# Kernel optimization log

Measured on AMD Instinct MI355X. Metric: run time of the kernel, lower is better.

Reference implementation:

```python
import jax, jax.numpy as jnp
import numpy as np
from jax import lax

WIN = 9
EPS = 1e-05


def _box_sum(v, win):
    # v: [B, 1, D, H, W]
    pad = win // 2
    dn = lax.conv_dimension_numbers(v.shape, (1, 1, win, win, win), ('NCDHW', 'OIDHW', 'NCDHW'))
    k = jnp.ones((win,), v.dtype)
    # apply 1D sum along D, H, W in turn
    v = lax.conv_general_dilated(v, k.reshape(1, 1, win, 1, 1), (1, 1, 1), [(pad, pad), (0, 0), (0, 0)], dimension_numbers=dn)
    v = lax.conv_general_dilated(v, k.reshape(1, 1, 1, win, 1), (1, 1, 1), [(0, 0), (pad, pad), (0, 0)], dimension_numbers=dn)
    v = lax.conv_general_dilated(v, k.reshape(1, 1, 1, 1, win), (1, 1, 1), [(0, 0), (0, 0), (pad, pad)], dimension_numbers=dn)
    return v


def setup_inputs() -> dict:
    key = jax.random.key(0)
    k1, k2 = jax.random.split(key)
    shape = (2, 1, 160, 192, 160)
    x = jax.random.uniform(k1, shape, dtype=jnp.float32)
    y = jax.random.uniform(k2, shape, dtype=jnp.float32)
    return {"x": x, "y": y}


def reference(x, y):
    win = WIN
    win_size = float(win ** 3)
    x_sum = _box_sum(x, win)
    y_sum = _box_sum(y, win)
    x2_sum = _box_sum(x * x, win)
    y2_sum = _box_sum(y * y, win)
    xy_sum = _box_sum(x * y, win)
    cross = xy_sum - x_sum * y_sum / win_size
    x_var = jnp.maximum(x2_sum - x_sum * x_sum / win_size, EPS)
    y_var = jnp.maximum(y2_sum - y_sum * y_sum / win_size, EPS)
    cc = cross * cross / (x_var * y_var)
    return -jnp.mean(cc)
```

## Files before the change

kernel.cpp:

```cpp
#include <hip/hip_runtime.h>

#define BB 2
#define DD 160
#define HH 192
#define WW 160
#define HW (HH * WW)
#define PAD 4
#define TH 16
#define TW 16
#define EXT 24
#define XSTR 28
#define PLANE 768
#define SLOTS (EXT * XSTR)
#define WCS 456
#define WJS 28
#define HCS 272
#define HHS 17
#define CHUNK 28
#define NCH 6
#define NITER 36
#define WT (WW / TW)
#define HT (HH / TH)
#define NBLK (WT * HT * NCH * BB)
#define EPS 1e-5f
#define INV_WS (1.0f / 729.0f)

__device__ __forceinline__ void bar_lgkm() {
  asm volatile("s_waitcnt lgkmcnt(0)" ::: "memory");
  __builtin_amdgcn_s_barrier();
  asm volatile("" ::: "memory");
}

__global__ void __launch_bounds__(256) k_lncc(
    const float* __restrict__ x, const float* __restrict__ y,
    float* __restrict__ partials)
{
  __shared__ float sbuf[2][2][PLANE];
  __shared__ float wsum[5 * WCS];
  __shared__ float hsum[5 * HCS];
  __shared__ float red[4];

  const int t = threadIdx.x;
  const int w0 = blockIdx.x * TW;
  const int h0 = blockIdx.y * TH;
  const int bz = blockIdx.z;
  const int b = bz / NCH;
  const int chunk = bz - b * NCH;
  const int dc0 = chunk * CHUNK;

  int off[3]; float msk[3];
#pragma unroll
  for (int k = 0; k < 3; ++k) {
    int s = t + 256 * k;
    int r = s / XSTR, cl = s - r * XSTR;
    int gh = h0 - PAD + r, gw = w0 - PAD + cl;
    bool ok = (s < SLOTS) & (cl < EXT) &
              ((unsigned)gh < (unsigned)HH) & ((unsigned)gw < (unsigned)WW);
    off[k] = ok ? (gh * WW + gw) : 0;
    msk[k] = ok ? 1.0f : 0.0f;
  }

  const int c2 = t / 24, r2 = t - c2 * 24;
  const bool aIsY = (c2 == 1) | (c2 == 3);
  const bool bIsX = (c2 == 2);
  const bool useB = (c2 >= 2);
  const int paOff = (aIsY ? PLANE : 0) + r2 * XSTR;
  const int pbOff = (bIsX ? 0 : PLANE) + r2 * XSTR;
  float* const wwr = &wsum[c2 * WCS + r2];

  const int c3 = t / 16, w3 = t - c3 * 16;
  const float* const wrd = &wsum[c3 * WCS + w3 * WJS];
  float* const hwr = &hsum[c3 * HCS + w3];

  const int h4 = t >> 4, w4 = t & 15;
  const float* const hrd = &hsum[h4 * HHS + w4];

  const float* xb = x + (long)b * DD * HW;
  const float* yb = y + (long)b * DD * HW;

  float ring[9][5];
#pragma unroll
  for (int i = 0; i < 9; ++i)
#pragma unroll
    for (int c = 0; c < 5; ++c) ring[i][c] = 0.f;
  float run0 = 0.f, run1 = 0.f, run2 = 0.f, run3 = 0.f, run4 = 0.f, acc = 0.f;

  const int g0 = dc0 - PAD;

  float vx0 = 0.f, vx1 = 0.f, vx2 = 0.f, vy0 = 0.f, vy1 = 0.f, vy2 = 0.f;
  if (g0 >= 0) {
    const float* xsl = xb + (long)g0 * HW;
    const float* ysl = yb + (long)g0 * HW;
    vx0 = xsl[off[0]]; vx1 = xsl[off[1]]; vx2 = xsl[off[2]];
    vy0 = ysl[off[0]]; vy1 = ysl[off[1]]; vy2 = ysl[off[2]];
  }

  for (int ito = 0; ito < NITER; ito += 9) {
#pragma unroll
    for (int jj = 0; jj < 9; ++jj) {
      const int it = ito + jj;
      const int g = g0 + it;
      const int p = it & 1;
      const bool gv = (g >= 0) && (g < DD);
      float hv0 = 0.f, hv1 = 0.f, hv2 = 0.f, hv3 = 0.f, hv4 = 0.f;

      if (gv) {
        float* xd = &sbuf[p][0][0];
        float* yd = &sbuf[p][1][0];
        xd[t]       = vx0 * msk[0];
        yd[t]       = vy0 * msk[0];
        xd[t + 256] = vx1 * msk[1];
        yd[t + 256] = vy1 * msk[1];
        xd[t + 512] = vx2 * msk[2];
        yd[t + 512] = vy2 * msk[2];
      }
      {
        const int gn = g + 1;
        if ((gn >= 0) && (gn < DD) && (it + 1 < NITER)) {
          const float* xsl = xb + (long)gn * HW;
          const float* ysl = yb + (long)gn * HW;
          vx0 = xsl[off[0]]; vx1 = xsl[off[1]]; vx2 = xsl[off[2]];
          vy0 = ysl[off[0]]; vy1 = ysl[off[1]]; vy2 = ysl[off[2]];
        }
      }

      if (gv) {
        bar_lgkm();
        if (t < 120) {
          const int pbase = p * (2 * PLANE);
          const float* pa = &sbuf[0][0][0] + pbase + paOff;
          const float* pb = &sbuf[0][0][0] + pbase + pbOff;
          float q[EXT];
#pragma unroll
          for (int i = 0; i < EXT; ++i) {
            float a = pa[i];
            float bv = pb[i];
            q[i] = useB ? a * bv : a;
          }
          float s = ((q[0] + q[1]) + (q[2] + q[3])) +
                    ((q[4] + q[5]) + (q[6] + q[7])) + q[8];
          wwr[0] = s;
#pragma unroll
          for (int j = 1; j < TW; ++j) {
            s += q[j + 8] - q[j - 1];
            wwr[j * WJS] = s;
          }
        }
        bar_lgkm();
        if (t < 80) {
          float v[EXT];
#pragma unroll
          for (int i = 0; i < EXT; ++i) v[i] = wrd[i];
          float s = ((v[0] + v[1]) + (v[2] + v[3])) +
                    ((v[4] + v[5]) + (v[6] + v[7])) + v[8];
          hwr[0] = s;
#pragma unroll
          for (int h = 1; h < TH; ++h) {
            s += v[h + 8] - v[h - 1];
            hwr[h * HHS] = s;
          }
        }
        bar_lgkm();
        hv0 = hrd[0];
        hv1 = hrd[HCS];
        hv2 = hrd[2 * HCS];
        hv3 = hrd[3 * HCS];
        hv4 = hrd[4 * HCS];
      }

      run0 += hv0 - ring[jj][0]; ring[jj][0] = hv0;
      run1 += hv1 - ring[jj][1]; ring[jj][1] = hv1;
      run2 += hv2 - ring[jj][2]; ring[jj][2] = hv2;
      run3 += hv3 - ring[jj][3]; ring[jj][3] = hv3;
      run4 += hv4 - ring[jj][4]; ring[jj][4] = hv4;

      if (it >= 8) {
        const int d = g - PAD;
        if (d < DD) {
          float cross = fmaf(-run0 * INV_WS, run1, run4);
          float xv = fmaxf(fmaf(-run0 * INV_WS, run0, run2), EPS);
          float yv = fmaxf(fmaf(-run1 * INV_WS, run1, run3), EPS);
          acc += (cross * cross) * __builtin_amdgcn_rcpf(xv * yv);
        }
      }
    }
  }

#pragma unroll
  for (int o = 32; o > 0; o >>= 1) acc += __shfl_down(acc, o);
  if ((t & 63) == 0) red[t >> 6] = acc;
  __syncthreads();
  if (t == 0) {
    int bid = (bz * HT + blockIdx.y) * WT + blockIdx.x;
    partials[bid] = (red[0] + red[1]) + (red[2] + red[3]);
  }
}

__global__ void __launch_bounds__(256) k_finalize(
    const float* __restrict__ partials, float* __restrict__ out)
{
  __shared__ double red[256];
  double s = 0.0;
  for (int i = threadIdx.x; i < NBLK; i += 256) s += (double)partials[i];
  red[threadIdx.x] = s;
  __syncthreads();
  for (int o = 128; o > 0; o >>= 1) {
    if (threadIdx.x < o) red[threadIdx.x] += red[threadIdx.x + o];
    __syncthreads();
  }
  if (threadIdx.x == 0) {
    const double Nvox = (double)BB * DD * HH * WW;
    out[0] = (float)(-red[0] / Nvox);
  }
}

extern "C" void kernel_launch(void* const* d_in, const int* in_sizes, int n_in,
                              void* d_out, int out_size, void* d_ws, size_t ws_size,
                              hipStream_t stream) {
  (void)in_sizes; (void)n_in; (void)out_size; (void)ws_size;
  const float* x = (const float*)d_in[0];
  const float* y = (const float*)d_in[1];
  float* out = (float*)d_out;
  float* partials = (float*)d_ws;

  dim3 grid(WT, HT, BB * NCH);
  k_lncc<<<grid, 256, 0, stream>>>(x, y, partials);
  k_finalize<<<1, 256, 0, stream>>>(partials, out);
}
```

Baseline: 86.22 us.

## Process two depth slices per barrier round with float4 staging loads

Restructures the depth loop so each iteration handles two D-slices at once. The W-pass uses 240 threads and the H-pass 160 threads instead of 120 and 80, which halves the number of barrier rounds. Global loads become float4 vectorized, and a ones-buffer removes the per-thread branch between plain and product channels. Shared memory is merged into one aliased array and launch bounds request 4 blocks per CU. The cost is more LDS per block, more registers for dual staging, and more complex indexing.

```diff
diff --git a/kernel.cpp b/kernel.cpp
--- a/kernel.cpp
+++ b/kernel.cpp
@@ -10,15 +10,21 @@
 #define TW 16
 #define EXT 24
 #define XSTR 28
-#define PLANE 768
-#define SLOTS (EXT * XSTR)
-#define WCS 456
+#define PLW 672
+#define ONESB 2688
+#define WSB 2720
+#define WSS 2260
+#define WCS 452
 #define WJS 28
-#define HCS 272
+#define HSB 7240
+#define HSS 1365
+#define HCS 273
 #define HHS 17
+#define REDB 9972
+#define LWORDS 9984
 #define CHUNK 28
 #define NCH 6
-#define NITER 36
+#define NPAIR 18
 #define WT (WW / TW)
 #define HT (HH / TH)
 #define NBLK (WT * HT * NCH * BB)
@@ -31,14 +37,11 @@
   asm volatile("" ::: "memory");
 }
 
-__global__ void __launch_bounds__(256) k_lncc(
+__global__ void __launch_bounds__(256, 4) k_lncc(
     const float* __restrict__ x, const float* __restrict__ y,
     float* __restrict__ partials)
 {
-  __shared__ float sbuf[2][2][PLANE];
-  __shared__ float wsum[5 * WCS];
-  __shared__ float hsum[5 * HCS];
-  __shared__ float red[4];
+  __shared__ float L[LWORDS];
 
   const int t = threadIdx.x;
   const int w0 = blockIdx.x * TW;
@@ -47,36 +50,60 @@
   const int b = bz / NCH;
   const int chunk = bz - b * NCH;
   const int dc0 = chunk * CHUNK;
-
-  int off[3]; float msk[3];
-#pragma unroll
-  for (int k = 0; k < 3; ++k) {
-    int s = t + 256 * k;
-    int r = s / XSTR, cl = s - r * XSTR;
-    int gh = h0 - PAD + r, gw = w0 - PAD + cl;
-    bool ok = (s < SLOTS) & (cl < EXT) &
-              ((unsigned)gh < (unsigned)HH) & ((unsigned)gw < (unsigned)WW);
-    off[k] = ok ? (gh * WW + gw) : 0;
-    msk[k] = ok ? 1.0f : 0.0f;
-  }
-
-  const int c2 = t / 24, r2 = t - c2 * 24;
-  const bool aIsY = (c2 == 1) | (c2 == 3);
-  const bool bIsX = (c2 == 2);
-  const bool useB = (c2 >= 2);
-  const int paOff = (aIsY ? PLANE : 0) + r2 * XSTR;
-  const int pbOff = (bIsX ? 0 : PLANE) + r2 * XSTR;
-  float* const wwr = &wsum[c2 * WCS + r2];
-
-  const int c3 = t / 16, w3 = t - c3 * 16;
-  const float* const wrd = &wsum[c3 * WCS + w3 * WJS];
-  float* const hwr = &hsum[c3 * HCS + w3];
+  const int g0 = dc0 - PAD;
+
+  for (int i = t; i < WSB; i += 256) L[i] = (i >= ONESB) ? 1.0f : 0.0f;
+  __syncthreads();
+
+  int laddr0, laddr1, laddr2;
+  int tslc0, tslc1, tslc2;
+  bool tok0, tok1, tok2;
+  const float* gp0; const float* gp1; const float* gp2;
+  {
+    const float* bx = x + (long)b * DD * HW;
+    const float* by = y + (long)b * DD * HW;
+#define MKTASK(K, LA, TS, TK, GP)                                         \
+    {                                                                     \
+      int tau = t + 256 * K;                                              \
+      int s = tau / 288;                                                  \
+      int rem = tau - 288 * s;                                            \
+      int a = rem / 144;                                                  \
+      int rho = rem - 144 * a;                                            \
+      int r = rho / 6;                                                    \
+      int q = rho - 6 * r;                                                \
+      int gh = h0 - PAD + r;                                              \
+      int gw = w0 - PAD + 4 * q;                                          \
+      bool ok = (tau < 576) && ((unsigned)gh < (unsigned)HH) &&           \
+                ((unsigned)gw < (unsigned)WW);                            \
+      LA = ok ? ((2 * s + a) * PLW + r * XSTR + 4 * q) : 0;               \
+      TS = (s < 2) ? s : 0;                                               \
+      TK = ok;                                                            \
+      GP = (a ? by : bx) + (long)TS * HW + (ok ? (gh * WW + gw) : 0);     \
+    }
+    MKTASK(0, laddr0, tslc0, tok0, gp0)
+    MKTASK(1, laddr1, tslc1, tok1, gp1)
+    MKTASK(2, laddr2, tslc2, tok2, gp2)
+#undef MKTASK
+  }
+
+  const int s2 = (t >= 120) ? 1 : 0;
+  const int t2 = t - 120 * s2;
+  const int r2 = t2 / 5;
+  const int c2 = t2 - 5 * r2;
+  const int paOff = (2 * s2 + (((c2 == 1) || (c2 == 3)) ? 1 : 0)) * PLW + r2 * XSTR;
+  const int pbOff = (c2 < 2) ? ONESB
+                             : ((2 * s2 + ((c2 == 2) ? 0 : 1)) * PLW + r2 * XSTR);
+  const int wwOff = WSB + s2 * WSS + c2 * WCS + r2;
+
+  const int s3 = (t >= 80) ? 1 : 0;
+  const int t3 = t - 80 * s3;
+  const int w3 = t3 / 5;
+  const int c3 = t3 - 5 * w3;
+  const int rdOff = WSB + s3 * WSS + c3 * WCS + w3 * WJS;
+  const int hwOff = HSB + s3 * HSS + c3 * HCS + w3;
 
   const int h4 = t >> 4, w4 = t & 15;
-  const float* const hrd = &hsum[h4 * HHS + w4];
-
-  const float* xb = x + (long)b * DD * HW;
-  const float* yb = y + (long)b * DD * HW;
+  const int hrd = HSB + h4 * HHS + w4;
 
   float ring[9][5];
 #pragma unroll
@@ -85,114 +112,138 @@
     for (int c = 0; c < 5; ++c) ring[i][c] = 0.f;
   float run0 = 0.f, run1 = 0.f, run2 = 0.f, run3 = 0.f, run4 = 0.f, acc = 0.f;
 
-  const int g0 = dc0 - PAD;
-
-  float vx0 = 0.f, vx1 = 0.f, vx2 = 0.f, vy0 = 0.f, vy1 = 0.f, vy2 = 0.f;
-  if (g0 >= 0) {
-    const float* xsl = xb + (long)g0 * HW;
-    const float* ysl = yb + (long)g0 * HW;
-    vx0 = xsl[off[0]]; vx1 = xsl[off[1]]; vx2 = xsl[off[2]];
-    vy0 = ysl[off[0]]; vy1 = ysl[off[1]]; vy2 = ysl[off[2]];
-  }
-
-  for (int ito = 0; ito < NITER; ito += 9) {
-#pragma unroll
-    for (int jj = 0; jj < 9; ++jj) {
-      const int it = ito + jj;
-      const int g = g0 + it;
-      const int p = it & 1;
-      const bool gv = (g >= 0) && (g < DD);
-      float hv0 = 0.f, hv1 = 0.f, hv2 = 0.f, hv3 = 0.f, hv4 = 0.f;
-
-      if (gv) {
-        float* xd = &sbuf[p][0][0];
-        float* yd = &sbuf[p][1][0];
-        xd[t]       = vx0 * msk[0];
-        yd[t]       = vy0 * msk[0];
-        xd[t + 256] = vx1 * msk[1];
-        yd[t + 256] = vy1 * msk[1];
-        xd[t + 512] = vx2 * msk[2];
-        yd[t + 512] = vy2 * msk[2];
-      }
+  float4 stg0 = make_float4(0, 0, 0, 0), stg1 = stg0, stg2 = stg0;
+  bool pst0, pst1, pst2;
+  {
+    const bool v0 = ((unsigned)g0 < (unsigned)DD);
+    const bool v1 = ((unsigned)(g0 + 1) < (unsigned)DD);
+    const long off64 = (long)g0 * HW;
+    pst0 = tok0 && (tslc0 ? v1 : v0);
+    if (pst0) stg0 = *(const float4*)(gp0 + off64);
+    pst1 = tok1 && (tslc1 ? v1 : v0);
+    if (pst1) stg1 = *(const float4*)(gp1 + off64);
+    pst2 = tok2 && (tslc2 ? v1 : v0);
+    if (pst2) stg2 = *(const float4*)(gp2 + off64);
+  }
+
+  for (int o = 0; o < 2; ++o) {
+#pragma unroll
+    for (int j = 0; j < 9; ++j) {
+      const int kit = o * 9 + j;
+      const int gs0 = g0 + 2 * kit;
+      const bool gv0 = ((unsigned)gs0 < (unsigned)DD);
+      const bool gv1 = ((unsigned)(gs0 + 1) < (unsigned)DD);
+
+      if (pst0) *(float4*)&L[laddr0] = stg0;
+      if (pst1) *(float4*)&L[laddr1] = stg1;
+      if (pst2) *(float4*)&L[laddr2] = stg2;
+
       {
-        const int gn = g + 1;
-        if ((gn >= 0) && (gn < DD) && (it + 1 < NITER)) {
-          const float* xsl = xb + (long)gn * HW;
-          const float* ysl = yb + (long)gn * HW;
-          vx0 = xsl[off[0]]; vx1 = xsl[off[1]]; vx2 = xsl[off[2]];
-          vy0 = ysl[off[0]]; vy1 = ysl[off[1]]; vy2 = ysl[off[2]];
-        }
-      }
-
-      if (gv) {
+        const int gn = gs0 + 2;
+        const bool nv0 = ((unsigned)gn < (unsigned)DD) && (kit + 1 < NPAIR);
+        const bool nv1 = ((unsigned)(gn + 1) < (unsigned)DD) && (kit + 1 < NPAIR);
+        const long off64 = (long)gn * HW;
+        pst0 = tok0 && (tslc0 ? nv1 : nv0);
+        if (pst0) stg0 = *(const float4*)(gp0 + off64);
+        pst1 = tok1 && (tslc1 ? nv1 : nv0);
+        if (pst1) stg1 = *(const float4*)(gp1 + off64);
+        pst2 = tok2 && (tslc2 ? nv1 : nv0);
+        if (pst2) stg2 = *(const float4*)(gp2 + off64);
+      }
+
+      float h00 = 0.f, h01 = 0.f, h02 = 0.f, h03 = 0.f, h04 = 0.f;
+      float h10 = 0.f, h11 = 0.f, h12 = 0.f, h13 = 0.f, h14 = 0.f;
+
+      if (gv0 || gv1) {
         bar_lgkm();
-        if (t < 120) {
-          const int pbase = p * (2 * PLANE);
-          const float* pa = &sbuf[0][0][0] + pbase + paOff;
-          const float* pb = &sbuf[0][0][0] + pbase + pbOff;
-          float q[EXT];
-#pragma unroll
-          for (int i = 0; i < EXT; ++i) {
-            float a = pa[i];
-            float bv = pb[i];
-            q[i] = useB ? a * bv : a;
+        if (t < 240) {
+          const bool gvs = s2 ? gv1 : gv0;
+          if (gvs) {
+            const float* pa = &L[paOff];
+            const float* pb = &L[pbOff];
+            float qv[EXT];
+#pragma unroll
+            for (int i = 0; i < EXT; ++i) qv[i] = pa[i] * pb[i];
+            float s = ((qv[0] + qv[1]) + (qv[2] + qv[3])) +
+                      ((qv[4] + qv[5]) + (qv[6] + qv[7])) + qv[8];
+            L[wwOff] = s;
+#pragma unroll
+            for (int jj = 1; jj < TW; ++jj) {
+              s += qv[jj + 8] - qv[jj - 1];
+              L[wwOff + jj * WJS] = s;
+            }
           }
-          float s = ((q[0] + q[1]) + (q[2] + q[3])) +
-                    ((q[4] + q[5]) + (q[6] + q[7])) + q[8];
-          wwr[0] = s;
-#pragma unroll
-          for (int j = 1; j < TW; ++j) {
-            s += q[j + 8] - q[j - 1];
-            wwr[j * WJS] = s;
+        }
+        bar_lgkm();
+        if (t < 160) {
+          const bool gvs = s3 ? gv1 : gv0;
+          if (gvs) {
+            const float* v = &L[rdOff];
+            float vv[EXT];
+#pragma unroll
+            for (int i = 0; i < EXT; ++i) vv[i] = v[i];
+            float s = ((vv[0] + vv[1]) + (vv[2] + vv[3])) +
+                      ((vv[4] + vv[5]) + (vv[6] + vv[7])) + vv[8];
+            L[hwOff] = s;
+#pragma unroll
+            for (int hh = 1; hh < TH; ++hh) {
+              s += vv[hh + 8] - vv[hh - 1];
+              L[hwOff + hh * HHS] = s;
+            }
           }
         }
         bar_lgkm();
-        if (t < 80) {
-          float v[EXT];
-#pragma unroll
-          for (int i = 0; i < EXT; ++i) v[i] = wrd[i];
-          float s = ((v[0] + v[1]) + (v[2] + v[3])) +
-                    ((v[4] + v[5]) + (v[6] + v[7])) + v[8];
-          hwr[0] = s;
-#pragma unroll
-          for (int h = 1; h < TH; ++h) {
-            s += v[h + 8] - v[h - 1];
-            hwr[h * HHS] = s;
-          }
-        }
-        bar_lgkm();
-        hv0 = hrd[0];
-        hv1 = hrd[HCS];
-        hv2 = hrd[2 * HCS];
-        hv3 = hrd[3 * HCS];
-        hv4 = hrd[4 * HCS];
-      }
-
-      run0 += hv0 - ring[jj][0]; ring[jj][0] = hv0;
-      run1 += hv1 - ring[jj][1]; ring[jj][1] = hv1;
-      run2 += hv2 - ring[jj][2]; ring[jj][2] = hv2;
-      run3 += hv3 - ring[jj][3]; ring[jj][3] = hv3;
-      run4 += hv4 - ring[jj][4]; ring[jj][4] = hv4;
-
-      if (it >= 8) {
-        const int d = g - PAD;
-        if (d < DD) {
+        if (gv0) {
+          h00 = L[hrd];           h01 = L[hrd + HCS];     h02 = L[hrd + 2 * HCS];
+          h03 = L[hrd + 3 * HCS]; h04 = L[hrd + 4 * HCS];
+        }
+        if (gv1) {
+          h10 = L[hrd + HSS];           h11 = L[hrd + HSS + HCS];
+          h12 = L[hrd + HSS + 2 * HCS]; h13 = L[hrd + HSS + 3 * HCS];
+          h14 = L[hrd + HSS + 4 * HCS];
+        }
+      }
+
+      {
+        const int ra = (2 * j) % 9;
+        run0 += h00 - ring[ra][0]; ring[ra][0] = h00;
+        run1 += h01 - ring[ra][1]; ring[ra][1] = h01;
+        run2 += h02 - ring[ra][2]; ring[ra][2] = h02;
+        run3 += h03 - ring[ra][3]; ring[ra][3] = h03;
+        run4 += h04 - ring[ra][4]; ring[ra][4] = h04;
+        const int d0v = gs0 - PAD;
+        if (d0v >= dc0 && d0v < DD) {
           float cross = fmaf(-run0 * INV_WS, run1, run4);
           float xv = fmaxf(fmaf(-run0 * INV_WS, run0, run2), EPS);
           float yv = fmaxf(fmaf(-run1 * INV_WS, run1, run3), EPS);
           acc += (cross * cross) * __builtin_amdgcn_rcpf(xv * yv);
         }
       }
+      {
+        const int rb = (2 * j + 1) % 9;
+        run0 += h10 - ring[rb][0]; ring[rb][0] = h10;
+        run1 += h11 - ring[rb][1]; ring[rb][1] = h11;
+        run2 += h12 - ring[rb][2]; ring[rb][2] = h12;
+        run3 += h13 - ring[rb][3]; ring[rb][3] = h13;
+        run4 += h14 - ring[rb][4]; ring[rb][4] = h14;
+        const int d1v = gs0 + 1 - PAD;
+        if (d1v >= dc0 && d1v < DD) {
+          float cross = fmaf(-run0 * INV_WS, run1, run4);
+          float xv = fmaxf(fmaf(-run0 * INV_WS, run0, run2), EPS);
+          float yv = fmaxf(fmaf(-run1 * INV_WS, run1, run3), EPS);
+          acc += (cross * cross) * __builtin_amdgcn_rcpf(xv * yv);
+        }
+      }
     }
   }
 
 #pragma unroll
-  for (int o = 32; o > 0; o >>= 1) acc += __shfl_down(acc, o);
-  if ((t & 63) == 0) red[t >> 6] = acc;
+  for (int off2 = 32; off2 > 0; off2 >>= 1) acc += __shfl_down(acc, off2);
+  if ((t & 63) == 0) L[REDB + (t >> 6)] = acc;
   __syncthreads();
   if (t == 0) {
     int bid = (bz * HT + blockIdx.y) * WT + blockIdx.x;
-    partials[bid] = (red[0] + red[1]) + (red[2] + red[3]);
+    partials[bid] = (L[REDB] + L[REDB + 1]) + (L[REDB + 2] + L[REDB + 3]);
   }
 }
 
```

New measurement: 108.3 us. +25.6%, slower.

## Compute W-direction box sums in registers from float4 global loads

Applied to the files above, without the earlier changes.

Drops the raw x/y shared-memory staging plane. Each of 96 threads now loads three float4 segments of a row directly from global memory and computes the five W-direction sliding sums for four output columns in registers, writing them to shared memory as float4. This removes one barrier per slice and the scalar LDS staging traffic. In exchange it does redundant global reads, since each thread fetches 12 values to produce 4 outputs. Boundary masking now happens per float4, which relies on the 16-aligned tile and the padding of 4.

```diff
diff --git a/kernel.cpp b/kernel.cpp
--- a/kernel.cpp
+++ b/kernel.cpp
@@ -8,14 +8,11 @@
 #define PAD 4
 #define TH 16
 #define TW 16
-#define EXT 24
-#define XSTR 28
-#define PLANE 768
-#define SLOTS (EXT * XSTR)
-#define WCS 456
-#define WJS 28
-#define HCS 272
-#define HHS 17
+#define EXTH 24
+#define WCS2 484
+#define WRS2 20
+#define HCS2 276
+#define HRS2 17
 #define CHUNK 28
 #define NCH 6
 #define NITER 36
@@ -35,9 +32,8 @@
     const float* __restrict__ x, const float* __restrict__ y,
     float* __restrict__ partials)
 {
-  __shared__ float sbuf[2][2][PLANE];
-  __shared__ float wsum[5 * WCS];
-  __shared__ float hsum[5 * HCS];
+  __shared__ __align__(16) float ws[5 * WCS2];
+  __shared__ __align__(16) float hs[5 * HCS2];
   __shared__ float red[4];
 
   const int t = threadIdx.x;
@@ -47,37 +43,31 @@
   const int b = bz / NCH;
   const int chunk = bz - b * NCH;
   const int dc0 = chunk * CHUNK;
-
-  int off[3]; float msk[3];
-#pragma unroll
-  for (int k = 0; k < 3; ++k) {
-    int s = t + 256 * k;
-    int r = s / XSTR, cl = s - r * XSTR;
-    int gh = h0 - PAD + r, gw = w0 - PAD + cl;
-    bool ok = (s < SLOTS) & (cl < EXT) &
-              ((unsigned)gh < (unsigned)HH) & ((unsigned)gw < (unsigned)WW);
-    off[k] = ok ? (gh * WW + gw) : 0;
-    msk[k] = ok ? 1.0f : 0.0f;
-  }
-
-  const int c2 = t / 24, r2 = t - c2 * 24;
-  const bool aIsY = (c2 == 1) | (c2 == 3);
-  const bool bIsX = (c2 == 2);
-  const bool useB = (c2 >= 2);
-  const int paOff = (aIsY ? PLANE : 0) + r2 * XSTR;
-  const int pbOff = (bIsX ? 0 : PLANE) + r2 * XSTR;
-  float* const wwr = &wsum[c2 * WCS + r2];
-
-  const int c3 = t / 16, w3 = t - c3 * 16;
-  const float* const wrd = &wsum[c3 * WCS + w3 * WJS];
-  float* const hwr = &hsum[c3 * HCS + w3];
-
-  const int h4 = t >> 4, w4 = t & 15;
-  const float* const hrd = &hsum[h4 * HHS + w4];
+  const int g0 = dc0 - PAD;
 
   const float* xb = x + (long)b * DD * HW;
   const float* yb = y + (long)b * DD * HW;
 
+  const int rA = t >> 2, g4 = t & 3;
+  const int gh = h0 - PAD + rA;
+  const int gw0 = w0 - PAD + 4 * g4;
+  const bool actA = (t < 96);
+  const bool rowOk = actA && ((unsigned)gh < (unsigned)HH);
+  const bool ok0 = rowOk && ((unsigned)gw0 < (unsigned)WW);
+  const bool ok1 = rowOk && ((unsigned)(gw0 + 4) < (unsigned)WW);
+  const bool ok2 = rowOk && ((unsigned)(gw0 + 8) < (unsigned)WW);
+  const int off0 = ok0 ? (gh * WW + gw0) : 0;
+  const int off1 = ok1 ? (gh * WW + gw0 + 4) : 0;
+  const int off2 = ok2 ? (gh * WW + gw0 + 8) : 0;
+  const int wbaseA = rA * WRS2 + 4 * g4;
+
+  const int cB = t >> 4, wB = t & 15;
+  const float* const rbB = &ws[cB * WCS2 + wB];
+  float* const hbB = &hs[cB * HCS2 + wB];
+
+  const int h4 = t >> 4, w4 = t & 15;
+  const float* const hrC = &hs[h4 * HRS2 + w4];
+
   float ring[9][5];
 #pragma unroll
   for (int i = 0; i < 9; ++i)
@@ -85,87 +75,88 @@
     for (int c = 0; c < 5; ++c) ring[i][c] = 0.f;
   float run0 = 0.f, run1 = 0.f, run2 = 0.f, run3 = 0.f, run4 = 0.f, acc = 0.f;
 
-  const int g0 = dc0 - PAD;
-
-  float vx0 = 0.f, vx1 = 0.f, vx2 = 0.f, vy0 = 0.f, vy1 = 0.f, vy2 = 0.f;
-  if (g0 >= 0) {
-    const float* xsl = xb + (long)g0 * HW;
-    const float* ysl = yb + (long)g0 * HW;
-    vx0 = xsl[off[0]]; vx1 = xsl[off[1]]; vx2 = xsl[off[2]];
-    vy0 = ysl[off[0]]; vy1 = ysl[off[1]]; vy2 = ysl[off[2]];
-  }
-
-  for (int ito = 0; ito < NITER; ito += 9) {
+  const float4 z4 = make_float4(0.f, 0.f, 0.f, 0.f);
+  float4 cx0 = z4, cx1 = z4, cx2 = z4, cy0 = z4, cy1 = z4, cy2 = z4;
+  if ((unsigned)g0 < (unsigned)DD) {
+    const long so = (long)g0 * HW;
+    cx0 = ok0 ? *(const float4*)(xb + so + off0) : z4;
+    cx1 = ok1 ? *(const float4*)(xb + so + off1) : z4;
+    cx2 = ok2 ? *(const float4*)(xb + so + off2) : z4;
+    cy0 = ok0 ? *(const float4*)(yb + so + off0) : z4;
+    cy1 = ok1 ? *(const float4*)(yb + so + off1) : z4;
+    cy2 = ok2 ? *(const float4*)(yb + so + off2) : z4;
+  }
+
+  for (int ko = 0; ko < 4; ++ko) {
 #pragma unroll
     for (int jj = 0; jj < 9; ++jj) {
-      const int it = ito + jj;
-      const int g = g0 + it;
-      const int p = it & 1;
-      const bool gv = (g >= 0) && (g < DD);
-      float hv0 = 0.f, hv1 = 0.f, hv2 = 0.f, hv3 = 0.f, hv4 = 0.f;
-
-      if (gv) {
-        float* xd = &sbuf[p][0][0];
-        float* yd = &sbuf[p][1][0];
-        xd[t]       = vx0 * msk[0];
-        yd[t]       = vy0 * msk[0];
-        xd[t + 256] = vx1 * msk[1];
-        yd[t + 256] = vy1 * msk[1];
-        xd[t + 512] = vx2 * msk[2];
-        yd[t + 512] = vy2 * msk[2];
-      }
+      const int k = ko * 9 + jj;
+      const int g = g0 + k;
+      const bool gv = ((unsigned)g < (unsigned)DD);
+
+      if (gv && actA) {
+        float xa[12], ya[12];
+        xa[0]=cx0.x; xa[1]=cx0.y; xa[2]=cx0.z; xa[3]=cx0.w;
+        xa[4]=cx1.x; xa[5]=cx1.y; xa[6]=cx1.z; xa[7]=cx1.w;
+        xa[8]=cx2.x; xa[9]=cx2.y; xa[10]=cx2.z; xa[11]=cx2.w;
+        ya[0]=cy0.x; ya[1]=cy0.y; ya[2]=cy0.z; ya[3]=cy0.w;
+        ya[4]=cy1.x; ya[5]=cy1.y; ya[6]=cy1.z; ya[7]=cy1.w;
+        ya[8]=cy2.x; ya[9]=cy2.y; ya[10]=cy2.z; ya[11]=cy2.w;
+#define EMITCH(CIDX, EXPR)                                                 \
+        {                                                                  \
+          float qv[12];                                                    \
+          _Pragma("unroll")                                                \
+          for (int i = 0; i < 12; ++i) qv[i] = (EXPR);                     \
+          float o0 = ((qv[0]+qv[1])+(qv[2]+qv[3]))+                        \
+                     ((qv[4]+qv[5])+(qv[6]+qv[7]))+qv[8];                  \
+          float o1 = o0 + qv[9]  - qv[0];                                  \
+          float o2 = o1 + qv[10] - qv[1];                                  \
+          float o3 = o2 + qv[11] - qv[2];                                  \
+          *(float4*)&ws[(CIDX) * WCS2 + wbaseA] = make_float4(o0,o1,o2,o3);\
+        }
+        EMITCH(0, xa[i])
+        EMITCH(1, ya[i])
+        EMITCH(2, xa[i] * xa[i])
+        EMITCH(3, ya[i] * ya[i])
+        EMITCH(4, xa[i] * ya[i])
+#undef EMITCH
+      }
+
+      float4 nx0 = z4, nx1 = z4, nx2 = z4, ny0 = z4, ny1 = z4, ny2 = z4;
       {
         const int gn = g + 1;
-        if ((gn >= 0) && (gn < DD) && (it + 1 < NITER)) {
-          const float* xsl = xb + (long)gn * HW;
-          const float* ysl = yb + (long)gn * HW;
-          vx0 = xsl[off[0]]; vx1 = xsl[off[1]]; vx2 = xsl[off[2]];
-          vy0 = ysl[off[0]]; vy1 = ysl[off[1]]; vy2 = ysl[off[2]];
-        }
-      }
-
+        const bool nv = (k + 1 < NITER) && ((unsigned)gn < (unsigned)DD);
+        const long so = (long)gn * HW;
+        nx0 = (ok0 && nv) ? *(const float4*)(xb + so + off0) : z4;
+        nx1 = (ok1 && nv) ? *(const float4*)(xb + so + off1) : z4;
+        nx2 = (ok2 && nv) ? *(const float4*)(xb + so + off2) : z4;
+        ny0 = (ok0 && nv) ? *(const float4*)(yb + so + off0) : z4;
+        ny1 = (ok1 && nv) ? *(const float4*)(yb + so + off1) : z4;
+        ny2 = (ok2 && nv) ? *(const float4*)(yb + so + off2) : z4;
+      }
+
+      float hv0 = 0.f, hv1 = 0.f, hv2 = 0.f, hv3 = 0.f, hv4 = 0.f;
       if (gv) {
         bar_lgkm();
-        if (t < 120) {
-          const int pbase = p * (2 * PLANE);
-          const float* pa = &sbuf[0][0][0] + pbase + paOff;
-          const float* pb = &sbuf[0][0][0] + pbase + pbOff;
-          float q[EXT];
-#pragma unroll
-          for (int i = 0; i < EXT; ++i) {
-            float a = pa[i];
-            float bv = pb[i];
-            q[i] = useB ? a * bv : a;
-          }
-          float s = ((q[0] + q[1]) + (q[2] + q[3])) +
-                    ((q[4] + q[5]) + (q[6] + q[7])) + q[8];
-          wwr[0] = s;
-#pragma unroll
-          for (int j = 1; j < TW; ++j) {
-            s += q[j + 8] - q[j - 1];
-            wwr[j * WJS] = s;
+        if (t < 80) {
+          float v[EXTH];
+#pragma unroll
+          for (int i = 0; i < EXTH; ++i) v[i] = rbB[i * WRS2];
+          float s = ((v[0] + v[1]) + (v[2] + v[3])) +
+                    ((v[4] + v[5]) + (v[6] + v[7])) + v[8];
+          hbB[0] = s;
+#pragma unroll
+          for (int h = 1; h < TH; ++h) {
+            s += v[h + 8] - v[h - 1];
+            hbB[h * HRS2] = s;
           }
         }
         bar_lgkm();
-        if (t < 80) {
-          float v[EXT];
-#pragma unroll
-          for (int i = 0; i < EXT; ++i) v[i] = wrd[i];
-          float s = ((v[0] + v[1]) + (v[2] + v[3])) +
-                    ((v[4] + v[5]) + (v[6] + v[7])) + v[8];
-          hwr[0] = s;
-#pragma unroll
-          for (int h = 1; h < TH; ++h) {
-            s += v[h + 8] - v[h - 1];
-            hwr[h * HHS] = s;
-          }
-        }
-        bar_lgkm();
-        hv0 = hrd[0];
-        hv1 = hrd[HCS];
-        hv2 = hrd[2 * HCS];
-        hv3 = hrd[3 * HCS];
-        hv4 = hrd[4 * HCS];
+        hv0 = hrC[0];
+        hv1 = hrC[HCS2];
+        hv2 = hrC[2 * HCS2];
+        hv3 = hrC[3 * HCS2];
+        hv4 = hrC[4 * HCS2];
       }
 
       run0 += hv0 - ring[jj][0]; ring[jj][0] = hv0;
@@ -174,8 +165,8 @@
       run3 += hv3 - ring[jj][3]; ring[jj][3] = hv3;
       run4 += hv4 - ring[jj][4]; ring[jj][4] = hv4;
 
-      if (it >= 8) {
-        const int d = g - PAD;
+      if (k >= 8) {
+        const int d = dc0 + (k - 8);
         if (d < DD) {
           float cross = fmaf(-run0 * INV_WS, run1, run4);
           float xv = fmaxf(fmaf(-run0 * INV_WS, run0, run2), EPS);
@@ -183,6 +174,9 @@
           acc += (cross * cross) * __builtin_amdgcn_rcpf(xv * yv);
         }
       }
+
+      cx0 = nx0; cx1 = nx1; cx2 = nx2;
+      cy0 = ny0; cy1 = ny1; cy2 = ny2;
     }
   }
 
```

After: 130.3 us. 51.2% more time.
